# Optimization experiments

Measured on AMD Instinct MI355X. Metric: run time of the kernel, lower is better.

The kernel has to match this reference:

```python
import jax, jax.numpy as jnp
import numpy as np

N_NODES = 50000
N_EDGES = 600000
IN_DIM = 128
HID = 128


def setup_inputs() -> dict:
    key = jax.random.key(0)
    ks = jax.random.split(key, 8)
    x = jax.random.normal(ks[0], (N_NODES, IN_DIM), dtype=jnp.float32)
    edge_index = jax.random.randint(ks[1], (2, N_EDGES), 0, N_NODES, dtype=jnp.int64)
    def lin(k, fan_in, fan_out):
        s = 1.0 / np.sqrt(fan_in)
        kw, kb = jax.random.split(k)
        W = jax.random.uniform(kw, (fan_in, fan_out), jnp.float32, -s, s)
        b = jax.random.uniform(kb, (fan_out,), jnp.float32, -s, s)
        return W, b
    W0, b0 = lin(ks[2], IN_DIM, HID)
    W1, b1 = lin(ks[3], HID, HID)
    W2, b2 = lin(ks[4], HID, HID)
    return {"x": x, "edge_index": edge_index, "W0": W0, "b0": b0,
            "W1": W1, "b1": b1, "W2": W2, "b2": b2}


def reference(x, edge_index, W0, b0, W1, b1, W2, b2):
    n = x.shape[0]
    loops = jnp.arange(n, dtype=edge_index.dtype)
    src = jnp.concatenate([edge_index[0], loops])  # source nodes (+self loops)
    dst = jnp.concatenate([edge_index[1], loops])  # destination nodes
    # symmetric GCN normalization: deg^{-1/2}[src] * deg^{-1/2}[dst]
    deg = jax.ops.segment_sum(jnp.ones(src.shape[0], x.dtype), dst, num_segments=n)
    dinv = jnp.where(deg > 0, jax.lax.rsqrt(deg), 0.0)
    norm = dinv[src] * dinv[dst]  # [E+N]

    def gcn_layer(h, W, b):
        hw = h @ W                              # [N, H]
        msg = hw[src] * norm[:, None]           # gather + scale, [E+N, H]
        agg = jax.ops.segment_sum(msg, dst, num_segments=n)  # scatter-add
        return agg + b

    h = x
    for W, b in ((W0, b0), (W1, b1), (W2, b2)):
        h = jax.nn.relu(gcn_layer(h, W, b))     # dropout is identity in eval
    return h  # JK='last'
```

## Files before the change

kernel.cpp:

```cpp
#include <hip/hip_runtime.h>

#define NN 50000
#define NE 600000
#define DIM 128
#define NB_N 196
#define NB_E 2344
#define TILES 3125
#define ROWW 136
#define NEPAD (NE + 3 * NN + 4096)

typedef unsigned short u16;
typedef unsigned int u32;
typedef __attribute__((ext_vector_type(8))) short bf16x8;
typedef __attribute__((ext_vector_type(4))) float f32x4;

__device__ __forceinline__ u16 f2bf(float f) {
    u32 u = __builtin_bit_cast(u32, f);
    u32 r = (u + 0x7FFFu + ((u >> 16) & 1u)) >> 16;
    return (u16)r;
}
__device__ __forceinline__ float bflo(u32 w) { return __builtin_bit_cast(float, w << 16); }
__device__ __forceinline__ float bfhi(u32 w) { return __builtin_bit_cast(float, w & 0xffff0000u); }


__global__ __launch_bounds__(256) void k_count(const int* __restrict__ ei,
                                               int* __restrict__ deg) {
    __shared__ int s64;
    if (threadIdx.x == 0) {
        int o = 0;
#pragma unroll
        for (int j = 0; j < 16; j++) o |= ei[2 * j + 1];
        s64 = (o == 0);
    }
    __syncthreads();
    int e = blockIdx.x * 256 + threadIdx.x;
    if (e >= NE) return;
    int d = s64 ? ei[2 * (NE + e)] : ei[NE + e];
    atomicAdd(&deg[d], 1);
}

__global__ __launch_bounds__(256) void k_scanA(const int* __restrict__ deg,
                                               int* __restrict__ rp4,
                                               int* __restrict__ bsum) {
    __shared__ int buf[256];
    int t = threadIdx.x, i = blockIdx.x * 256 + t;
    int v = (i < NN) ? ((deg[i] + 3) & ~3) : 0;
    buf[t] = v;
    __syncthreads();
    for (int off = 1; off < 256; off <<= 1) {
        int x = (t >= off) ? buf[t - off] : 0;
        __syncthreads();
        buf[t] += x;
        __syncthreads();
    }
    if (i < NN) rp4[i] = buf[t] - v;
    if (t == 255) bsum[blockIdx.x] = buf[255];
}

__global__ __launch_bounds__(256) void k_scanB(int* __restrict__ bsum) {
    __shared__ int buf[256];
    int t = threadIdx.x;
    int v = (t < NB_N) ? bsum[t] : 0;
    buf[t] = v;
    __syncthreads();
    for (int off = 1; off < 256; off <<= 1) {
        int x = (t >= off) ? buf[t - off] : 0;
        __syncthreads();
        buf[t] += x;
        __syncthreads();
    }
    bsum[t] = buf[t] - v;
}

__global__ __launch_bounds__(256) void k_scanC(const int* __restrict__ deg,
                                               int* __restrict__ rp4,
                                               const int* __restrict__ bsum,
                                               float* __restrict__ dinv) {
    int i = blockIdx.x * 256 + threadIdx.x;
    if (i < NN) {
        rp4[i] += bsum[i >> 8];
        dinv[i] = rsqrtf((float)(deg[i] + 1));
    }
    if (i == 0) rp4[NN] = bsum[255];
}

__global__ __launch_bounds__(256) void k_fill(const int* __restrict__ ei,
                                              const int* __restrict__ rp4,
                                              int* __restrict__ cursor,
                                              const float* __restrict__ dinv,
                                              int* __restrict__ csr_src,
                                              float* __restrict__ csr_norm) {
    __shared__ int s64;
    if (threadIdx.x == 0) {
        int o = 0;
#pragma unroll
        for (int j = 0; j < 16; j++) o |= ei[2 * j + 1];
        s64 = (o == 0);
    }
    __syncthreads();
    int e = blockIdx.x * 256 + threadIdx.x;
    if (e >= NE) return;
    int is64 = s64;
    int s = is64 ? ei[2 * e] : ei[e];
    int d = is64 ? ei[2 * (NE + e)] : ei[NE + e];
    int pos = rp4[d] + atomicAdd(&cursor[d], 1);
    csr_src[pos] = s;
    csr_norm[pos] = dinv[s] * dinv[d];
}

__global__ __launch_bounds__(256) void k_wcast(const float* __restrict__ W0,
                                               const float* __restrict__ W1,
                                               const float* __restrict__ W2,
                                               u16* __restrict__ Wt) {
    int idx = blockIdx.x * 256 + threadIdx.x;
    int l = idx >> 14, rem = idx & 16383;
    int n = rem >> 7, k = rem & 127;
    const float* W = (l == 0) ? W0 : ((l == 1) ? W1 : W2);
    Wt[idx] = f2bf(W[k * 128 + n]);
}

__global__ __launch_bounds__(256) void k_gemm_f32(const float* __restrict__ x,
                                                  const u16* __restrict__ Wt,
                                                  u16* __restrict__ hwb) {
    int lane = threadIdx.x & 63;
    int tile = blockIdx.x * 4 + (threadIdx.x >> 6);
    if (tile >= TILES) return;
    int r = lane & 15, q = lane >> 4;

    bf16x8 Bf[8][4];
#pragma unroll
    for (int nt = 0; nt < 8; nt++)
#pragma unroll
        for (int kc = 0; kc < 4; kc++)
            Bf[nt][kc] = *(const bf16x8*)(Wt + ((nt * 16 + r) << 7) + kc * 32 + q * 8);

    long rowbase = (long)tile * 16;
    bf16x8 Af[4];
#pragma unroll
    for (int kc = 0; kc < 4; kc++) {
        const float4* p = (const float4*)(x + (rowbase + r) * 128 + kc * 32 + q * 8);
        float4 t0 = p[0], t1 = p[1];
        bf16x8 a;
        a[0] = (short)f2bf(t0.x); a[1] = (short)f2bf(t0.y);
        a[2] = (short)f2bf(t0.z); a[3] = (short)f2bf(t0.w);
        a[4] = (short)f2bf(t1.x); a[5] = (short)f2bf(t1.y);
        a[6] = (short)f2bf(t1.z); a[7] = (short)f2bf(t1.w);
        Af[kc] = a;
    }

#pragma unroll
    for (int nt = 0; nt < 8; nt++) {
        f32x4 acc = {0.f, 0.f, 0.f, 0.f};
#pragma unroll
        for (int kc = 0; kc < 4; kc++)
            acc = __builtin_amdgcn_mfma_f32_16x16x32_bf16(Af[kc], Bf[nt][kc], acc, 0, 0, 0);
#pragma unroll
        for (int i = 0; i < 4; i++)
            hwb[(rowbase + q * 4 + i) * 128 + nt * 16 + r] = f2bf(acc[i]);
    }
}

__device__ __forceinline__ void fma8(float* acc, uint4 u, float n) {
    acc[0] += n * bflo(u.x); acc[1] += n * bfhi(u.x);
    acc[2] += n * bflo(u.y); acc[3] += n * bfhi(u.y);
    acc[4] += n * bflo(u.z); acc[5] += n * bfhi(u.z);
    acc[6] += n * bflo(u.w); acc[7] += n * bfhi(u.w);
}

__device__ __forceinline__ void agg_node16(const u16* __restrict__ hw,
                                           const int* __restrict__ rp4,
                                           const int* __restrict__ cs,
                                           const float* __restrict__ cn,
                                           const float* __restrict__ bias,
                                           float dv, int v, int g, int r,
                                           float* acc) {
    uint4 sv = *(const uint4*)(hw + (size_t)v * DIM + r * 8);
    float sc = (g == 0) ? dv * dv : 0.0f;
    acc[0] = sc * bflo(sv.x); acc[1] = sc * bfhi(sv.x);
    acc[2] = sc * bflo(sv.y); acc[3] = sc * bfhi(sv.y);
    acc[4] = sc * bflo(sv.z); acc[5] = sc * bfhi(sv.z);
    acc[6] = sc * bflo(sv.w); acc[7] = sc * bfhi(sv.w);
    int e = rp4[v], end = rp4[v + 1];
    for (; e + 8 <= end; e += 8) {
        int s0 = cs[e + g], s1 = cs[e + 4 + g];
        float n0 = cn[e + g], n1 = cn[e + 4 + g];
        uint4 u0 = *(const uint4*)(hw + (size_t)s0 * DIM + r * 8);
        uint4 u1 = *(const uint4*)(hw + (size_t)s1 * DIM + r * 8);
        fma8(acc, u0, n0);
        fma8(acc, u1, n1);
    }
    if (e < end) {
        int s0 = cs[e + g];
        float n0 = cn[e + g];
        uint4 u0 = *(const uint4*)(hw + (size_t)s0 * DIM + r * 8);
        fma8(acc, u0, n0);
    }
#pragma unroll
    for (int j = 0; j < 8; j++) {
        acc[j] += __shfl_xor(acc[j], 16, 64);
        acc[j] += __shfl_xor(acc[j], 32, 64);
    }
    float4 b0 = ((const float4*)bias)[2 * r];
    float4 b1 = ((const float4*)bias)[2 * r + 1];
    acc[0] = fmaxf(acc[0] + b0.x, 0.f); acc[1] = fmaxf(acc[1] + b0.y, 0.f);
    acc[2] = fmaxf(acc[2] + b0.z, 0.f); acc[3] = fmaxf(acc[3] + b0.w, 0.f);
    acc[4] = fmaxf(acc[4] + b1.x, 0.f); acc[5] = fmaxf(acc[5] + b1.y, 0.f);
    acc[6] = fmaxf(acc[6] + b1.z, 0.f); acc[7] = fmaxf(acc[7] + b1.w, 0.f);
}

__global__ __launch_bounds__(256) void k_agg_gemm(const u16* __restrict__ hw_in,
                                                  const int* __restrict__ rp4,
                                                  const int* __restrict__ cs,
                                                  const float* __restrict__ cn,
                                                  const float* __restrict__ dinv,
                                                  const float* __restrict__ bias,
                                                  const u16* __restrict__ Wt,
                                                  u16* __restrict__ hw_out) {
    __shared__ u16 sm[16 * ROWW];
    int lane = threadIdx.x & 63;
    int w = threadIdx.x >> 6;
    int g = lane >> 4, r = lane & 15;
    int base = blockIdx.x * 16;
#pragma unroll
    for (int ni = 0; ni < 4; ni++) {
        int row = w * 4 + ni, v = base + row;
        float acc[8];
        agg_node16(hw_in, rp4, cs, cn, bias, dinv[v], v, g, r, acc);
        if (g == 0) {
            uint4 p;
            p.x = (u32)f2bf(acc[0]) | ((u32)f2bf(acc[1]) << 16);
            p.y = (u32)f2bf(acc[2]) | ((u32)f2bf(acc[3]) << 16);
            p.z = (u32)f2bf(acc[4]) | ((u32)f2bf(acc[5]) << 16);
            p.w = (u32)f2bf(acc[6]) | ((u32)f2bf(acc[7]) << 16);
            *(uint4*)(sm + row * ROWW + r * 8) = p;
        }
    }
    __syncthreads();
    int q = lane >> 4;
    bf16x8 Af[4];
#pragma unroll
    for (int kc = 0; kc < 4; kc++)
        Af[kc] = *(const bf16x8*)(sm + r * ROWW + kc * 32 + q * 8);
#pragma unroll
    for (int t = 0; t < 2; t++) {
        int nt = w * 2 + t;
        f32x4 acc = {0.f, 0.f, 0.f, 0.f};
#pragma unroll
        for (int kc = 0; kc < 4; kc++) {
            bf16x8 Bf = *(const bf16x8*)(Wt + ((nt * 16 + r) << 7) + kc * 32 + q * 8);
            acc = __builtin_amdgcn_mfma_f32_16x16x32_bf16(Af[kc], Bf, acc, 0, 0, 0);
        }
#pragma unroll
        for (int i = 0; i < 4; i++)
            hw_out[(size_t)(base + q * 4 + i) * DIM + nt * 16 + r] = f2bf(acc[i]);
    }
}

__global__ __launch_bounds__(256) void k_agg_out(const u16* __restrict__ hw_in,
                                                 const int* __restrict__ rp4,
                                                 const int* __restrict__ cs,
                                                 const float* __restrict__ cn,
                                                 const float* __restrict__ dinv,
                                                 const float* __restrict__ bias,
                                                 float* __restrict__ out) {
    int lane = threadIdx.x & 63;
    int w = threadIdx.x >> 6;
    int g = lane >> 4, r = lane & 15;
    int v = blockIdx.x * 4 + w;
    float acc[8];
    agg_node16(hw_in, rp4, cs, cn, bias, dinv[v], v, g, r, acc);
    if (g == 0) {
        float4 o0 = {acc[0], acc[1], acc[2], acc[3]};
        float4 o1 = {acc[4], acc[5], acc[6], acc[7]};
        float4* p = (float4*)(out + (size_t)v * DIM + r * 8);
        p[0] = o0;
        p[1] = o1;
    }
}


extern "C" void kernel_launch(void* const* d_in, const int* in_sizes, int n_in,
                              void* d_out, int out_size, void* d_ws, size_t ws_size,
                              hipStream_t stream) {
    const float* x = (const float*)d_in[0];
    const int* ei = (const int*)d_in[1];
    const float* W0 = (const float*)d_in[2];
    const float* b0 = (const float*)d_in[3];
    const float* W1 = (const float*)d_in[4];
    const float* b1 = (const float*)d_in[5];
    const float* W2 = (const float*)d_in[6];
    const float* b2 = (const float*)d_in[7];

    char* ws = (char*)d_ws;
    size_t off = 0;
    auto alloc = [&](size_t bytes) -> void* {
        void* p = ws + off;
        off += (bytes + 511) & ~(size_t)511;
        return p;
    };
    int* deg = (int*)alloc(NN * 4);
    int* cursor = (int*)alloc(NN * 4);
    int* csr_src = (int*)alloc((size_t)NEPAD * 4);
    float* csr_norm = (float*)alloc((size_t)NEPAD * 4);
    size_t zbytes = off;
    float* dinv = (float*)alloc(NN * 4);
    int* rp4 = (int*)alloc((NN + 1) * 4);
    int* bsum = (int*)alloc(256 * 4);
    u16* Wt = (u16*)alloc(3 * 128 * 128 * 2);
    u16* hwA = (u16*)alloc((size_t)NN * DIM * 2);
    u16* hwB = (u16*)alloc((size_t)NN * DIM * 2);

    hipMemsetAsync(ws, 0, zbytes, stream);
    k_count<<<NB_E, 256, 0, stream>>>(ei, deg);
    k_scanA<<<NB_N, 256, 0, stream>>>(deg, rp4, bsum);
    k_scanB<<<1, 256, 0, stream>>>(bsum);
    k_scanC<<<NB_N, 256, 0, stream>>>(deg, rp4, bsum, dinv);
    k_fill<<<NB_E, 256, 0, stream>>>(ei, rp4, cursor, dinv, csr_src, csr_norm);
    k_wcast<<<192, 256, 0, stream>>>(W0, W1, W2, Wt);

    k_gemm_f32<<<(TILES + 3) / 4, 256, 0, stream>>>(x, Wt, hwA);
    k_agg_gemm<<<TILES, 256, 0, stream>>>(hwA, rp4, csr_src, csr_norm,
                                          dinv, b0, Wt + 16384, hwB);
    k_agg_gemm<<<TILES, 256, 0, stream>>>(hwB, rp4, csr_src, csr_norm,
                                          dinv, b1, Wt + 32768, hwA);
    k_agg_out<<<NN / 4, 256, 0, stream>>>(hwA, rp4, csr_src, csr_norm,
                                          dinv, b2, (float*)d_out);
}
```

Measured before the change: 281.4 us.

## Interleave CSR src/norm records, pad rows to 8, and aggregate node pairs with prefetch

Edge source index and normalization are packed into one int2 record array, so each lane loads two edges with a single 16-byte load instead of separate index and norm loads. Row padding moves from 4 to 8 (at least 8 per node), which removes the tail branch. Each wave now aggregates two nodes at once and software-prefetches the next record batch to raise memory-level parallelism. The cost is more padded zero-weight gathers, a larger record footprint and higher register pressure from two accumulator sets.

```diff
diff --git a/kernel.cpp b/kernel.cpp
--- a/kernel.cpp
+++ b/kernel.cpp
@@ -7,7 +7,7 @@
 #define NB_E 2344
 #define TILES 3125
 #define ROWW 136
-#define NEPAD (NE + 3 * NN + 4096)
+#define NEPAD (NE + 8 * NN + 64)
 
 typedef unsigned short u16;
 typedef unsigned int u32;
@@ -21,6 +21,7 @@
 }
 __device__ __forceinline__ float bflo(u32 w) { return __builtin_bit_cast(float, w << 16); }
 __device__ __forceinline__ float bfhi(u32 w) { return __builtin_bit_cast(float, w & 0xffff0000u); }
+__device__ __forceinline__ float i2f(int b) { return __builtin_bit_cast(float, b); }
 
 
 __global__ __launch_bounds__(256) void k_count(const int* __restrict__ ei,
@@ -40,11 +41,15 @@
 }
 
 __global__ __launch_bounds__(256) void k_scanA(const int* __restrict__ deg,
-                                               int* __restrict__ rp4,
+                                               int* __restrict__ rp8,
                                                int* __restrict__ bsum) {
     __shared__ int buf[256];
     int t = threadIdx.x, i = blockIdx.x * 256 + t;
-    int v = (i < NN) ? ((deg[i] + 3) & ~3) : 0;
+    int v = 0;
+    if (i < NN) {
+        v = (deg[i] + 7) & ~7;
+        if (v == 0) v = 8;
+    }
     buf[t] = v;
     __syncthreads();
     for (int off = 1; off < 256; off <<= 1) {
@@ -53,7 +58,7 @@
         buf[t] += x;
         __syncthreads();
     }
-    if (i < NN) rp4[i] = buf[t] - v;
+    if (i < NN) rp8[i] = buf[t] - v;
     if (t == 255) bsum[blockIdx.x] = buf[255];
 }
 
@@ -73,23 +78,22 @@
 }
 
 __global__ __launch_bounds__(256) void k_scanC(const int* __restrict__ deg,
-                                               int* __restrict__ rp4,
+                                               int* __restrict__ rp8,
                                                const int* __restrict__ bsum,
                                                float* __restrict__ dinv) {
     int i = blockIdx.x * 256 + threadIdx.x;
     if (i < NN) {
-        rp4[i] += bsum[i >> 8];
+        rp8[i] += bsum[i >> 8];
         dinv[i] = rsqrtf((float)(deg[i] + 1));
     }
-    if (i == 0) rp4[NN] = bsum[255];
+    if (i == 0) rp8[NN] = bsum[255];
 }
 
 __global__ __launch_bounds__(256) void k_fill(const int* __restrict__ ei,
-                                              const int* __restrict__ rp4,
+                                              const int* __restrict__ rp8,
                                               int* __restrict__ cursor,
                                               const float* __restrict__ dinv,
-                                              int* __restrict__ csr_src,
-                                              float* __restrict__ csr_norm) {
+                                              int2* __restrict__ recs) {
     __shared__ int s64;
     if (threadIdx.x == 0) {
         int o = 0;
@@ -103,9 +107,11 @@
     int is64 = s64;
     int s = is64 ? ei[2 * e] : ei[e];
     int d = is64 ? ei[2 * (NE + e)] : ei[NE + e];
-    int pos = rp4[d] + atomicAdd(&cursor[d], 1);
-    csr_src[pos] = s;
-    csr_norm[pos] = dinv[s] * dinv[d];
+    int pos = rp8[d] + atomicAdd(&cursor[d], 1);
+    int2 rc;
+    rc.x = s;
+    rc.y = __builtin_bit_cast(int, dinv[s] * dinv[d]);
+    recs[pos] = rc;
 }
 
 __global__ __launch_bounds__(256) void k_wcast(const float* __restrict__ W0,
@@ -167,34 +173,18 @@
     acc[6] += n * bflo(u.w); acc[7] += n * bfhi(u.w);
 }
 
-__device__ __forceinline__ void agg_node16(const u16* __restrict__ hw,
-                                           const int* __restrict__ rp4,
-                                           const int* __restrict__ cs,
-                                           const float* __restrict__ cn,
-                                           const float* __restrict__ bias,
-                                           float dv, int v, int g, int r,
-                                           float* acc) {
+__device__ __forceinline__ void self_init(const u16* hw, float dv, int v, int g,
+                                          int r, float* acc) {
     uint4 sv = *(const uint4*)(hw + (size_t)v * DIM + r * 8);
     float sc = (g == 0) ? dv * dv : 0.0f;
     acc[0] = sc * bflo(sv.x); acc[1] = sc * bfhi(sv.x);
     acc[2] = sc * bflo(sv.y); acc[3] = sc * bfhi(sv.y);
     acc[4] = sc * bflo(sv.z); acc[5] = sc * bfhi(sv.z);
     acc[6] = sc * bflo(sv.w); acc[7] = sc * bfhi(sv.w);
-    int e = rp4[v], end = rp4[v + 1];
-    for (; e + 8 <= end; e += 8) {
-        int s0 = cs[e + g], s1 = cs[e + 4 + g];
-        float n0 = cn[e + g], n1 = cn[e + 4 + g];
-        uint4 u0 = *(const uint4*)(hw + (size_t)s0 * DIM + r * 8);
-        uint4 u1 = *(const uint4*)(hw + (size_t)s1 * DIM + r * 8);
-        fma8(acc, u0, n0);
-        fma8(acc, u1, n1);
-    }
-    if (e < end) {
-        int s0 = cs[e + g];
-        float n0 = cn[e + g];
-        uint4 u0 = *(const uint4*)(hw + (size_t)s0 * DIM + r * 8);
-        fma8(acc, u0, n0);
-    }
+}
+
+__device__ __forceinline__ void combine_bias_relu(const float* bias, int r,
+                                                  float* acc) {
 #pragma unroll
     for (int j = 0; j < 8; j++) {
         acc[j] += __shfl_xor(acc[j], 16, 64);
@@ -208,10 +198,41 @@
     acc[6] = fmaxf(acc[6] + b1.z, 0.f); acc[7] = fmaxf(acc[7] + b1.w, 0.f);
 }
 
+__device__ __forceinline__ void agg_pair(const u16* __restrict__ hw,
+                                         const int* __restrict__ rp8,
+                                         const int2* __restrict__ recs,
+                                         const float* __restrict__ dinv,
+                                         int va, int vb, int g, int r,
+                                         float* A, float* B) {
+    self_init(hw, dinv[va], va, g, r, A);
+    self_init(hw, dinv[vb], vb, g, r, B);
+    int ea = rp8[va], enda = rp8[va + 1];
+    int eb = rp8[vb], endb = rp8[vb + 1];
+    int4 qa = *(const int4*)(recs + ea + 2 * g);
+    int4 qb = *(const int4*)(recs + eb + 2 * g);
+    while (ea < enda || eb < endb) {
+        float na0 = (ea < enda) ? i2f(qa.y) : 0.f;
+        float na1 = (ea < enda) ? i2f(qa.w) : 0.f;
+        float nb0 = (eb < endb) ? i2f(qb.y) : 0.f;
+        float nb1 = (eb < endb) ? i2f(qb.w) : 0.f;
+        uint4 ua0 = *(const uint4*)(hw + (size_t)(u32)qa.x * DIM + r * 8);
+        uint4 ua1 = *(const uint4*)(hw + (size_t)(u32)qa.z * DIM + r * 8);
+        uint4 ub0 = *(const uint4*)(hw + (size_t)(u32)qb.x * DIM + r * 8);
+        uint4 ub1 = *(const uint4*)(hw + (size_t)(u32)qb.z * DIM + r * 8);
+        ea += 8; eb += 8;
+        int pa = min(ea, enda - 8);
+        int pb = min(eb, endb - 8);
+        int4 qa_n = *(const int4*)(recs + pa + 2 * g);
+        int4 qb_n = *(const int4*)(recs + pb + 2 * g);
+        fma8(A, ua0, na0); fma8(A, ua1, na1);
+        fma8(B, ub0, nb0); fma8(B, ub1, nb1);
+        qa = qa_n; qb = qb_n;
+    }
+}
+
 __global__ __launch_bounds__(256) void k_agg_gemm(const u16* __restrict__ hw_in,
-                                                  const int* __restrict__ rp4,
-                                                  const int* __restrict__ cs,
-                                                  const float* __restrict__ cn,
+                                                  const int* __restrict__ rp8,
+                                                  const int2* __restrict__ recs,
                                                   const float* __restrict__ dinv,
                                                   const float* __restrict__ bias,
                                                   const u16* __restrict__ Wt,
@@ -222,17 +243,25 @@
     int g = lane >> 4, r = lane & 15;
     int base = blockIdx.x * 16;
 #pragma unroll
-    for (int ni = 0; ni < 4; ni++) {
-        int row = w * 4 + ni, v = base + row;
-        float acc[8];
-        agg_node16(hw_in, rp4, cs, cn, bias, dinv[v], v, g, r, acc);
+    for (int p = 0; p < 2; p++) {
+        int rowa = w * 4 + 2 * p;
+        int va = base + rowa;
+        float A[8], B[8];
+        agg_pair(hw_in, rp8, recs, dinv, va, va + 1, g, r, A, B);
+        combine_bias_relu(bias, r, A);
+        combine_bias_relu(bias, r, B);
         if (g == 0) {
-            uint4 p;
-            p.x = (u32)f2bf(acc[0]) | ((u32)f2bf(acc[1]) << 16);
-            p.y = (u32)f2bf(acc[2]) | ((u32)f2bf(acc[3]) << 16);
-            p.z = (u32)f2bf(acc[4]) | ((u32)f2bf(acc[5]) << 16);
-            p.w = (u32)f2bf(acc[6]) | ((u32)f2bf(acc[7]) << 16);
-            *(uint4*)(sm + row * ROWW + r * 8) = p;
+            uint4 pk;
+            pk.x = (u32)f2bf(A[0]) | ((u32)f2bf(A[1]) << 16);
+            pk.y = (u32)f2bf(A[2]) | ((u32)f2bf(A[3]) << 16);
+            pk.z = (u32)f2bf(A[4]) | ((u32)f2bf(A[5]) << 16);
+            pk.w = (u32)f2bf(A[6]) | ((u32)f2bf(A[7]) << 16);
+            *(uint4*)(sm + rowa * ROWW + r * 8) = pk;
+            pk.x = (u32)f2bf(B[0]) | ((u32)f2bf(B[1]) << 16);
+            pk.y = (u32)f2bf(B[2]) | ((u32)f2bf(B[3]) << 16);
+            pk.z = (u32)f2bf(B[4]) | ((u32)f2bf(B[5]) << 16);
+            pk.w = (u32)f2bf(B[6]) | ((u32)f2bf(B[7]) << 16);
+            *(uint4*)(sm + (rowa + 1) * ROWW + r * 8) = pk;
         }
     }
     __syncthreads();
@@ -257,24 +286,26 @@
 }
 
 __global__ __launch_bounds__(256) void k_agg_out(const u16* __restrict__ hw_in,
-                                                 const int* __restrict__ rp4,
-                                                 const int* __restrict__ cs,
-                                                 const float* __restrict__ cn,
+                                                 const int* __restrict__ rp8,
+                                                 const int2* __restrict__ recs,
                                                  const float* __restrict__ dinv,
                                                  const float* __restrict__ bias,
                                                  float* __restrict__ out) {
     int lane = threadIdx.x & 63;
     int w = threadIdx.x >> 6;
     int g = lane >> 4, r = lane & 15;
-    int v = blockIdx.x * 4 + w;
-    float acc[8];
-    agg_node16(hw_in, rp4, cs, cn, bias, dinv[v], v, g, r, acc);
+    int va = blockIdx.x * 8 + w * 2;
+    float A[8], B[8];
+    agg_pair(hw_in, rp8, recs, dinv, va, va + 1, g, r, A, B);
+    combine_bias_relu(bias, r, A);
+    combine_bias_relu(bias, r, B);
     if (g == 0) {
-        float4 o0 = {acc[0], acc[1], acc[2], acc[3]};
-        float4 o1 = {acc[4], acc[5], acc[6], acc[7]};
-        float4* p = (float4*)(out + (size_t)v * DIM + r * 8);
-        p[0] = o0;
-        p[1] = o1;
+        float4* p = (float4*)(out + (size_t)va * DIM + r * 8);
+        p[0] = make_float4(A[0], A[1], A[2], A[3]);
+        p[1] = make_float4(A[4], A[5], A[6], A[7]);
+        p = (float4*)(out + (size_t)(va + 1) * DIM + r * 8);
+        p[0] = make_float4(B[0], B[1], B[2], B[3]);
+        p[1] = make_float4(B[4], B[5], B[6], B[7]);
     }
 }
 
@@ -300,11 +331,10 @@
     };
     int* deg = (int*)alloc(NN * 4);
     int* cursor = (int*)alloc(NN * 4);
-    int* csr_src = (int*)alloc((size_t)NEPAD * 4);
-    float* csr_norm = (float*)alloc((size_t)NEPAD * 4);
+    int2* recs = (int2*)alloc((size_t)NEPAD * 8);
     size_t zbytes = off;
     float* dinv = (float*)alloc(NN * 4);
-    int* rp4 = (int*)alloc((NN + 1) * 4);
+    int* rp8 = (int*)alloc((NN + 1) * 4);
     int* bsum = (int*)alloc(256 * 4);
     u16* Wt = (u16*)alloc(3 * 128 * 128 * 2);
     u16* hwA = (u16*)alloc((size_t)NN * DIM * 2);
@@ -312,17 +342,17 @@
 
     hipMemsetAsync(ws, 0, zbytes, stream);
     k_count<<<NB_E, 256, 0, stream>>>(ei, deg);
-    k_scanA<<<NB_N, 256, 0, stream>>>(deg, rp4, bsum);
+    k_scanA<<<NB_N, 256, 0, stream>>>(deg, rp8, bsum);
     k_scanB<<<1, 256, 0, stream>>>(bsum);
-    k_scanC<<<NB_N, 256, 0, stream>>>(deg, rp4, bsum, dinv);
-    k_fill<<<NB_E, 256, 0, stream>>>(ei, rp4, cursor, dinv, csr_src, csr_norm);
+    k_scanC<<<NB_N, 256, 0, stream>>>(deg, rp8, bsum, dinv);
+    k_fill<<<NB_E, 256, 0, stream>>>(ei, rp8, cursor, dinv, recs);
     k_wcast<<<192, 256, 0, stream>>>(W0, W1, W2, Wt);
 
     k_gemm_f32<<<(TILES + 3) / 4, 256, 0, stream>>>(x, Wt, hwA);
-    k_agg_gemm<<<TILES, 256, 0, stream>>>(hwA, rp4, csr_src, csr_norm,
-                                          dinv, b0, Wt + 16384, hwB);
-    k_agg_gemm<<<TILES, 256, 0, stream>>>(hwB, rp4, csr_src, csr_norm,
-                                          dinv, b1, Wt + 32768, hwA);
-    k_agg_out<<<NN / 4, 256, 0, stream>>>(hwA, rp4, csr_src, csr_norm,
-                                          dinv, b2, (float*)d_out);
-}
+    k_agg_gemm<<<TILES, 256, 0, stream>>>(hwA, rp8, recs, dinv, b0,
+                                          Wt + 16384, hwB);
+    k_agg_gemm<<<TILES, 256, 0, stream>>>(hwB, rp8, recs, dinv, b1,
+                                          Wt + 32768, hwA);
+    k_agg_out<<<NN / 8, 256, 0, stream>>>(hwA, rp8, recs, dinv, b2,
+                                          (float*)d_out);
+}
```

New measurement: 277.9 us. No clear change (-1.2%).

## Interleave CSR src/norm records and aggregate four nodes per wave with prefetch

Applied to the files above, without the earlier changes.

CSR source indices and edge norms are packed into one int2 record array. Padding slots are zeroed in the scan instead of memsetting the whole edge buffer, and every node is padded to at least four edges. Aggregation now assigns one node to each 16-lane group, so a wave handles four nodes at once and prefetches the next records during the gathers. The aim is more memory-level parallelism and fewer index loads. The cost is uneven work across the wave when degrees differ, plus extra register pressure from the four-node accumulators.

```diff
diff --git a/kernel.cpp b/kernel.cpp
--- a/kernel.cpp
+++ b/kernel.cpp
@@ -7,7 +7,7 @@
 #define NB_E 2344
 #define TILES 3125
 #define ROWW 136
-#define NEPAD (NE + 3 * NN + 4096)
+#define NEPAD (NE + 4 * NN + 64)
 
 typedef unsigned short u16;
 typedef unsigned int u32;
@@ -21,6 +21,7 @@
 }
 __device__ __forceinline__ float bflo(u32 w) { return __builtin_bit_cast(float, w << 16); }
 __device__ __forceinline__ float bfhi(u32 w) { return __builtin_bit_cast(float, w & 0xffff0000u); }
+__device__ __forceinline__ float i2f(int b) { return __builtin_bit_cast(float, b); }
 
 
 __global__ __launch_bounds__(256) void k_count(const int* __restrict__ ei,
@@ -39,12 +40,17 @@
     atomicAdd(&deg[d], 1);
 }
 
+__device__ __forceinline__ int pad4(int d) {
+    int p = (d + 3) & ~3;
+    return p < 4 ? 4 : p;
+}
+
 __global__ __launch_bounds__(256) void k_scanA(const int* __restrict__ deg,
                                                int* __restrict__ rp4,
                                                int* __restrict__ bsum) {
     __shared__ int buf[256];
     int t = threadIdx.x, i = blockIdx.x * 256 + t;
-    int v = (i < NN) ? ((deg[i] + 3) & ~3) : 0;
+    int v = (i < NN) ? pad4(deg[i]) : 0;
     buf[t] = v;
     __syncthreads();
     for (int off = 1; off < 256; off <<= 1) {
@@ -75,11 +81,16 @@
 __global__ __launch_bounds__(256) void k_scanC(const int* __restrict__ deg,
                                                int* __restrict__ rp4,
                                                const int* __restrict__ bsum,
-                                               float* __restrict__ dinv) {
+                                               float* __restrict__ dinv,
+                                               int2* __restrict__ recs) {
     int i = blockIdx.x * 256 + threadIdx.x;
     if (i < NN) {
-        rp4[i] += bsum[i >> 8];
-        dinv[i] = rsqrtf((float)(deg[i] + 1));
+        int rp = rp4[i] + bsum[i >> 8];
+        rp4[i] = rp;
+        int d = deg[i];
+        dinv[i] = rsqrtf((float)(d + 1));
+        int p = pad4(d);
+        for (int j = d; j < p; j++) recs[rp + j] = make_int2(0, 0);
     }
     if (i == 0) rp4[NN] = bsum[255];
 }
@@ -88,8 +99,7 @@
                                               const int* __restrict__ rp4,
                                               int* __restrict__ cursor,
                                               const float* __restrict__ dinv,
-                                              int* __restrict__ csr_src,
-                                              float* __restrict__ csr_norm) {
+                                              int2* __restrict__ recs) {
     __shared__ int s64;
     if (threadIdx.x == 0) {
         int o = 0;
@@ -104,8 +114,10 @@
     int s = is64 ? ei[2 * e] : ei[e];
     int d = is64 ? ei[2 * (NE + e)] : ei[NE + e];
     int pos = rp4[d] + atomicAdd(&cursor[d], 1);
-    csr_src[pos] = s;
-    csr_norm[pos] = dinv[s] * dinv[d];
+    int2 rc;
+    rc.x = s;
+    rc.y = __builtin_bit_cast(int, dinv[s] * dinv[d]);
+    recs[pos] = rc;
 }
 
 __global__ __launch_bounds__(256) void k_wcast(const float* __restrict__ W0,
@@ -167,51 +179,74 @@
     acc[6] += n * bflo(u.w); acc[7] += n * bfhi(u.w);
 }
 
-__device__ __forceinline__ void agg_node16(const u16* __restrict__ hw,
-                                           const int* __restrict__ rp4,
-                                           const int* __restrict__ cs,
-                                           const float* __restrict__ cn,
-                                           const float* __restrict__ bias,
-                                           float dv, int v, int g, int r,
-                                           float* acc) {
-    uint4 sv = *(const uint4*)(hw + (size_t)v * DIM + r * 8);
-    float sc = (g == 0) ? dv * dv : 0.0f;
-    acc[0] = sc * bflo(sv.x); acc[1] = sc * bfhi(sv.x);
-    acc[2] = sc * bflo(sv.y); acc[3] = sc * bfhi(sv.y);
-    acc[4] = sc * bflo(sv.z); acc[5] = sc * bfhi(sv.z);
-    acc[6] = sc * bflo(sv.w); acc[7] = sc * bfhi(sv.w);
-    int e = rp4[v], end = rp4[v + 1];
-    for (; e + 8 <= end; e += 8) {
-        int s0 = cs[e + g], s1 = cs[e + 4 + g];
-        float n0 = cn[e + g], n1 = cn[e + 4 + g];
-        uint4 u0 = *(const uint4*)(hw + (size_t)s0 * DIM + r * 8);
-        uint4 u1 = *(const uint4*)(hw + (size_t)s1 * DIM + r * 8);
-        fma8(acc, u0, n0);
-        fma8(acc, u1, n1);
-    }
-    if (e < end) {
-        int s0 = cs[e + g];
-        float n0 = cn[e + g];
-        uint4 u0 = *(const uint4*)(hw + (size_t)s0 * DIM + r * 8);
-        fma8(acc, u0, n0);
-    }
+__device__ __forceinline__ void combine_bias_relu(float b0x, float b0y, float b0z,
+                                                  float b0w, float b1x, float b1y,
+                                                  float b1z, float b1w, float* acc) {
 #pragma unroll
     for (int j = 0; j < 8; j++) {
         acc[j] += __shfl_xor(acc[j], 16, 64);
         acc[j] += __shfl_xor(acc[j], 32, 64);
     }
-    float4 b0 = ((const float4*)bias)[2 * r];
-    float4 b1 = ((const float4*)bias)[2 * r + 1];
-    acc[0] = fmaxf(acc[0] + b0.x, 0.f); acc[1] = fmaxf(acc[1] + b0.y, 0.f);
-    acc[2] = fmaxf(acc[2] + b0.z, 0.f); acc[3] = fmaxf(acc[3] + b0.w, 0.f);
-    acc[4] = fmaxf(acc[4] + b1.x, 0.f); acc[5] = fmaxf(acc[5] + b1.y, 0.f);
-    acc[6] = fmaxf(acc[6] + b1.z, 0.f); acc[7] = fmaxf(acc[7] + b1.w, 0.f);
+    acc[0] = fmaxf(acc[0] + b0x, 0.f); acc[1] = fmaxf(acc[1] + b0y, 0.f);
+    acc[2] = fmaxf(acc[2] + b0z, 0.f); acc[3] = fmaxf(acc[3] + b0w, 0.f);
+    acc[4] = fmaxf(acc[4] + b1x, 0.f); acc[5] = fmaxf(acc[5] + b1y, 0.f);
+    acc[6] = fmaxf(acc[6] + b1z, 0.f); acc[7] = fmaxf(acc[7] + b1w, 0.f);
+}
+
+__device__ __forceinline__ void agg_quad(const u16* __restrict__ hw,
+                                         const int* __restrict__ rp4,
+                                         const int2* __restrict__ recs,
+                                         const float* __restrict__ dinv,
+                                         int vbase, int g, int r,
+                                         float A[4][8]) {
+    int4 rlo = *(const int4*)(rp4 + vbase);
+    int rhi = rp4[vbase + 4];
+    int s0 = rlo.x, s1 = rlo.y, s2 = rlo.z, s3 = rlo.w;
+    int l0 = rlo.y - rlo.x, l1 = rlo.z - rlo.y, l2 = rlo.w - rlo.z, l3 = rhi - rlo.w;
+
+    uint4 sv = *(const uint4*)(hw + (size_t)(vbase + g) * DIM + r * 8);
+    float4 dv4 = *(const float4*)(dinv + vbase);
+    float dvg = (g == 0) ? dv4.x : (g == 1) ? dv4.y : (g == 2) ? dv4.z : dv4.w;
+    float sc = dvg * dvg;
+
+    int2 q0 = recs[s0 + g], q1 = recs[s1 + g], q2 = recs[s2 + g], q3 = recs[s3 + g];
+
+#pragma unroll
+    for (int c = 0; c < 4; c++) {
+        float s = (g == c) ? sc : 0.f;
+        A[c][0] = s * bflo(sv.x); A[c][1] = s * bfhi(sv.x);
+        A[c][2] = s * bflo(sv.y); A[c][3] = s * bfhi(sv.y);
+        A[c][4] = s * bflo(sv.z); A[c][5] = s * bfhi(sv.z);
+        A[c][6] = s * bflo(sv.w); A[c][7] = s * bfhi(sv.w);
+    }
+
+    int nit = max(max(l0, l1), max(l2, l3)) >> 2;
+    for (int it = 0; it < nit; ++it) {
+        uint4 u0 = *(const uint4*)(hw + (size_t)(u32)q0.x * DIM + r * 8);
+        uint4 u1 = *(const uint4*)(hw + (size_t)(u32)q1.x * DIM + r * 8);
+        uint4 u2 = *(const uint4*)(hw + (size_t)(u32)q2.x * DIM + r * 8);
+        uint4 u3 = *(const uint4*)(hw + (size_t)(u32)q3.x * DIM + r * 8);
+        int nx = 4 * (it + 1);
+        int2 p0 = recs[s0 + min(nx, l0 - 4) + g];
+        int2 p1 = recs[s1 + min(nx, l1 - 4) + g];
+        int2 p2 = recs[s2 + min(nx, l2 - 4) + g];
+        int2 p3 = recs[s3 + min(nx, l3 - 4) + g];
+        int cur = 4 * it;
+        float n0 = (cur < l0) ? i2f(q0.y) : 0.f;
+        float n1 = (cur < l1) ? i2f(q1.y) : 0.f;
+        float n2 = (cur < l2) ? i2f(q2.y) : 0.f;
+        float n3 = (cur < l3) ? i2f(q3.y) : 0.f;
+        fma8(A[0], u0, n0);
+        fma8(A[1], u1, n1);
+        fma8(A[2], u2, n2);
+        fma8(A[3], u3, n3);
+        q0 = p0; q1 = p1; q2 = p2; q3 = p3;
+    }
 }
 
 __global__ __launch_bounds__(256) void k_agg_gemm(const u16* __restrict__ hw_in,
                                                   const int* __restrict__ rp4,
-                                                  const int* __restrict__ cs,
-                                                  const float* __restrict__ cn,
+                                                  const int2* __restrict__ recs,
                                                   const float* __restrict__ dinv,
                                                   const float* __restrict__ bias,
                                                   const u16* __restrict__ Wt,
@@ -221,18 +256,23 @@
     int w = threadIdx.x >> 6;
     int g = lane >> 4, r = lane & 15;
     int base = blockIdx.x * 16;
-#pragma unroll
-    for (int ni = 0; ni < 4; ni++) {
-        int row = w * 4 + ni, v = base + row;
-        float acc[8];
-        agg_node16(hw_in, rp4, cs, cn, bias, dinv[v], v, g, r, acc);
-        if (g == 0) {
-            uint4 p;
-            p.x = (u32)f2bf(acc[0]) | ((u32)f2bf(acc[1]) << 16);
-            p.y = (u32)f2bf(acc[2]) | ((u32)f2bf(acc[3]) << 16);
-            p.z = (u32)f2bf(acc[4]) | ((u32)f2bf(acc[5]) << 16);
-            p.w = (u32)f2bf(acc[6]) | ((u32)f2bf(acc[7]) << 16);
-            *(uint4*)(sm + row * ROWW + r * 8) = p;
+    int vbase = base + w * 4;
+
+    float4 b0 = ((const float4*)bias)[2 * r];
+    float4 b1 = ((const float4*)bias)[2 * r + 1];
+
+    float A[4][8];
+    agg_quad(hw_in, rp4, recs, dinv, vbase, g, r, A);
+#pragma unroll
+    for (int c = 0; c < 4; c++) {
+        combine_bias_relu(b0.x, b0.y, b0.z, b0.w, b1.x, b1.y, b1.z, b1.w, A[c]);
+        if (g == c) {
+            uint4 pk;
+            pk.x = (u32)f2bf(A[c][0]) | ((u32)f2bf(A[c][1]) << 16);
+            pk.y = (u32)f2bf(A[c][2]) | ((u32)f2bf(A[c][3]) << 16);
+            pk.z = (u32)f2bf(A[c][4]) | ((u32)f2bf(A[c][5]) << 16);
+            pk.w = (u32)f2bf(A[c][6]) | ((u32)f2bf(A[c][7]) << 16);
+            *(uint4*)(sm + (w * 4 + c) * ROWW + r * 8) = pk;
         }
     }
     __syncthreads();
@@ -258,23 +298,28 @@
 
 __global__ __launch_bounds__(256) void k_agg_out(const u16* __restrict__ hw_in,
                                                  const int* __restrict__ rp4,
-                                                 const int* __restrict__ cs,
-                                                 const float* __restrict__ cn,
+                                                 const int2* __restrict__ recs,
                                                  const float* __restrict__ dinv,
                                                  const float* __restrict__ bias,
                                                  float* __restrict__ out) {
     int lane = threadIdx.x & 63;
     int w = threadIdx.x >> 6;
     int g = lane >> 4, r = lane & 15;
-    int v = blockIdx.x * 4 + w;
-    float acc[8];
-    agg_node16(hw_in, rp4, cs, cn, bias, dinv[v], v, g, r, acc);
-    if (g == 0) {
-        float4 o0 = {acc[0], acc[1], acc[2], acc[3]};
-        float4 o1 = {acc[4], acc[5], acc[6], acc[7]};
-        float4* p = (float4*)(out + (size_t)v * DIM + r * 8);
-        p[0] = o0;
-        p[1] = o1;
+    int vbase = blockIdx.x * 16 + w * 4;
+
+    float4 b0 = ((const float4*)bias)[2 * r];
+    float4 b1 = ((const float4*)bias)[2 * r + 1];
+
+    float A[4][8];
+    agg_quad(hw_in, rp4, recs, dinv, vbase, g, r, A);
+#pragma unroll
+    for (int c = 0; c < 4; c++) {
+        combine_bias_relu(b0.x, b0.y, b0.z, b0.w, b1.x, b1.y, b1.z, b1.w, A[c]);
+        if (g == c) {
+            float4* p = (float4*)(out + (size_t)(vbase + c) * DIM + r * 8);
+            p[0] = make_float4(A[c][0], A[c][1], A[c][2], A[c][3]);
+            p[1] = make_float4(A[c][4], A[c][5], A[c][6], A[c][7]);
+        }
     }
 }
 
@@ -300,9 +345,8 @@
     };
     int* deg = (int*)alloc(NN * 4);
     int* cursor = (int*)alloc(NN * 4);
-    int* csr_src = (int*)alloc((size_t)NEPAD * 4);
-    float* csr_norm = (float*)alloc((size_t)NEPAD * 4);
     size_t zbytes = off;
+    int2* recs = (int2*)alloc((size_t)NEPAD * 8);
     float* dinv = (float*)alloc(NN * 4);
     int* rp4 = (int*)alloc((NN + 1) * 4);
     int* bsum = (int*)alloc(256 * 4);
@@ -314,15 +358,15 @@
     k_count<<<NB_E, 256, 0, stream>>>(ei, deg);
     k_scanA<<<NB_N, 256, 0, stream>>>(deg, rp4, bsum);
     k_scanB<<<1, 256, 0, stream>>>(bsum);
-    k_scanC<<<NB_N, 256, 0, stream>>>(deg, rp4, bsum, dinv);
-    k_fill<<<NB_E, 256, 0, stream>>>(ei, rp4, cursor, dinv, csr_src, csr_norm);
+    k_scanC<<<NB_N, 256, 0, stream>>>(deg, rp4, bsum, dinv, recs);
+    k_fill<<<NB_E, 256, 0, stream>>>(ei, rp4, cursor, dinv, recs);
     k_wcast<<<192, 256, 0, stream>>>(W0, W1, W2, Wt);
 
     k_gemm_f32<<<(TILES + 3) / 4, 256, 0, stream>>>(x, Wt, hwA);
-    k_agg_gemm<<<TILES, 256, 0, stream>>>(hwA, rp4, csr_src, csr_norm,
-                                          dinv, b0, Wt + 16384, hwB);
-    k_agg_gemm<<<TILES, 256, 0, stream>>>(hwB, rp4, csr_src, csr_norm,
-                                          dinv, b1, Wt + 32768, hwA);
-    k_agg_out<<<NN / 4, 256, 0, stream>>>(hwA, rp4, csr_src, csr_norm,
-                                          dinv, b2, (float*)d_out);
-}
+    k_agg_gemm<<<TILES, 256, 0, stream>>>(hwA, rp4, recs, dinv, b0,
+                                          Wt + 16384, hwB);
+    k_agg_gemm<<<TILES, 256, 0, stream>>>(hwB, rp4, recs, dinv, b1,
+                                          Wt + 32768, hwA);
+    k_agg_out<<<TILES, 256, 0, stream>>>(hwA, rp4, recs, dinv, b2,
+                                         (float*)d_out);
+}
```

After: 290.5 us. 3.2% more time.
